# Kernel optimization log

Hardware: AMD Instinct MI355X
Metric: run time of the kernel (lower is better)

The kernel has to match this reference:

```python
import jax, jax.numpy as jnp
import numpy as np

T, N, D, B, L = 4, 1_000_000, 4, 16_384, 50
TOTAL = B * L

def setup_inputs() -> dict:
    key = jax.random.key(0)
    k0, k1, k2, k3, k4 = jax.random.split(key, 5)
    tables = jax.random.normal(k0, (T, N, D), dtype=jnp.float32) * 0.01
    indices = jax.random.randint(k1, (T, TOTAL), 0, N)
    # sorted segment ids encode jagged bag boundaries (variable lengths per sample)
    segment_ids = jnp.sort(jax.random.randint(k2, (T, TOTAL), 0, B), axis=-1)
    W = jax.random.normal(k3, (1, D), dtype=jnp.float32) * (1.0 / np.sqrt(D))
    b = jax.random.normal(k4, (1,), dtype=jnp.float32) * 0.01
    return {"tables": tables, "W": W, "b": b, "indices": indices, "segment_ids": segment_ids}

def reference(tables, W, b, indices, segment_ids):
    # EmbeddingBagCollection: per-table gather + sum pooling over jagged bags
    def pool_one(tbl, idx, seg):
        rows = tbl[idx]                                   # [TOTAL, D] irregular gather
        return jax.ops.segment_sum(rows, seg, num_segments=B)  # [B, D]
    pooled = jax.vmap(pool_one)(tables, indices, segment_ids)  # [T, B, D]
    # to_dict() + per-key append + cat(dim=0)  ==  reshape stacking tables along batch
    sparse_features = pooled.reshape(T * B, D)            # [T*B, D]
    # over_arch Linear(4, 1)
    return sparse_features @ W.T + b                      # [T*B, 1]
```

## Files before the change

### kernel.cpp

```cpp
#include <hip/hip_runtime.h>

constexpr int T     = 4;
constexpr int NROWS = 1000000;
constexpr int B     = 16384;
constexpr int TOTAL = 16384 * 50;

typedef float fv4 __attribute__((ext_vector_type(4)));


__global__ __launch_bounds__(256)
void produce_kernel(const fv4*   __restrict__ tables,
                    const float* __restrict__ Wp,
                    const float* __restrict__ bias,
                    float* __restrict__ p,
                    float* __restrict__ out) {
    const int i = blockIdx.x * 256 + threadIdx.x;
    if (i < T * NROWS) {
        const float wx = Wp[0], wy = Wp[1], wz = Wp[2], ww = Wp[3];
        const fv4 r = tables[i];
        p[i] = r.x * wx + r.y * wy + r.z * wz + r.w * ww;
    }
    if (i < T * B) out[i] = bias[0];
}

__global__ __launch_bounds__(256)
void pool_kernel(const float* __restrict__ p,
                 const int*   __restrict__ indices,
                 const int*   __restrict__ segids,
                 float*       __restrict__ out)
{
    const int xcd    = blockIdx.x & 7;
    const int t      = xcd >> 1;
    const int within = (blockIdx.x >> 3) * 2 + (xcd & 1);
    const int local  = within * 256 + threadIdx.x;
    const int g      = t * TOTAL + local;

    const int lane = threadIdx.x & 63;

    const int seg = __builtin_nontemporal_load(&segids[g]);
    const int idx = __builtin_nontemporal_load(&indices[g]);
    float v = p[t * NROWS + idx];

    #pragma unroll
    for (int d = 1; d < 64; d <<= 1) {
        const float ov = __shfl_up(v, d, 64);
        const int   os = __shfl_up(seg, d, 64);
        if (lane >= d && os == seg) v += ov;
    }

    const int nseg = __shfl_down(seg, 1, 64);
    if (lane == 63 || nseg != seg) {
        atomicAdd(&out[t * B + seg], v);
    }
}

extern "C" void kernel_launch(void* const* d_in, const int* in_sizes, int n_in,
                              void* d_out, int out_size, void* d_ws, size_t ws_size,
                              hipStream_t stream) {
    const fv4*   tables  = (const fv4*)d_in[0];
    const float* W       = (const float*)d_in[1];
    const float* bias    = (const float*)d_in[2];
    const int*   indices = (const int*)d_in[3];
    const int*   segids  = (const int*)d_in[4];
    float*       out     = (float*)d_out;

    float* p = (float*)d_ws;

    {
        int n = T * NROWS;
        produce_kernel<<<(n + 255) / 256, 256, 0, stream>>>(tables, W, bias, p, out);
    }
    {
        pool_kernel<<<12800, 256, 0, stream>>>(p, indices, segids, out);
    }
}
```

Measured before the change: 133.5 us.

## Process four rows per thread in produce and four elements per thread in pool

The produce kernel now has each thread load four table rows with nontemporal 16-byte loads and write four projected values as one vector store. Its blocks use the same XCD-aware mapping from block to table as the pool kernel. The pool kernel reads indices and segment ids as int4 vectors and does a serial segmented prefix over its four elements. It then runs the wave-level shuffle scan on per-thread totals and carries the previous lane's sum into boundary atomics. The goal is fewer threads, wider memory transactions and fewer shuffle rounds per element, at the cost of more intricate carry logic and fewer resident waves to hide gather latency.

```diff
diff --git a/kernel.cpp b/kernel.cpp
--- a/kernel.cpp
+++ b/kernel.cpp
@@ -6,6 +6,7 @@
 constexpr int TOTAL = 16384 * 50;
 
 typedef float fv4 __attribute__((ext_vector_type(4)));
+typedef int   iv4 __attribute__((ext_vector_type(4)));
 
 
 __global__ __launch_bounds__(256)
@@ -14,44 +15,76 @@
                     const float* __restrict__ bias,
                     float* __restrict__ p,
                     float* __restrict__ out) {
-    const int i = blockIdx.x * 256 + threadIdx.x;
-    if (i < T * NROWS) {
+    const int xcd    = blockIdx.x & 7;
+    const int t      = xcd >> 1;
+    const int within = ((blockIdx.x >> 3) << 1) + (xcd & 1);
+    const int r0     = within * 1024 + threadIdx.x * 4;
+
+    if (r0 < NROWS) {
         const float wx = Wp[0], wy = Wp[1], wz = Wp[2], ww = Wp[3];
-        const fv4 r = tables[i];
-        p[i] = r.x * wx + r.y * wy + r.z * wz + r.w * ww;
+        const fv4* src = tables + t * NROWS + r0;
+        const fv4 a = __builtin_nontemporal_load(&src[0]);
+        const fv4 b = __builtin_nontemporal_load(&src[1]);
+        const fv4 c = __builtin_nontemporal_load(&src[2]);
+        const fv4 d = __builtin_nontemporal_load(&src[3]);
+        fv4 res;
+        res.x = a.x * wx + a.y * wy + a.z * wz + a.w * ww;
+        res.y = b.x * wx + b.y * wy + b.z * wz + b.w * ww;
+        res.z = c.x * wx + c.y * wy + c.z * wz + c.w * ww;
+        res.w = d.x * wx + d.y * wy + d.z * wz + d.w * ww;
+        *(fv4*)&p[t * NROWS + r0] = res;
     }
-    if (i < T * B) out[i] = bias[0];
+    const int flat = blockIdx.x * 256 + threadIdx.x;
+    if (flat < T * B) out[flat] = bias[0];
 }
 
 __global__ __launch_bounds__(256)
 void pool_kernel(const float* __restrict__ p,
-                 const int*   __restrict__ indices,
-                 const int*   __restrict__ segids,
+                 const iv4*   __restrict__ indices,
+                 const iv4*   __restrict__ segids,
                  float*       __restrict__ out)
 {
     const int xcd    = blockIdx.x & 7;
     const int t      = xcd >> 1;
-    const int within = (blockIdx.x >> 3) * 2 + (xcd & 1);
-    const int local  = within * 256 + threadIdx.x;
-    const int g      = t * TOTAL + local;
+    const int within = ((blockIdx.x >> 3) << 1) + (xcd & 1);
+    const int q      = within * 256 + threadIdx.x;
+    const int gq     = t * (TOTAL / 4) + q;
+    const int lane   = threadIdx.x & 63;
 
-    const int lane = threadIdx.x & 63;
+    const iv4 s4 = __builtin_nontemporal_load(&segids[gq]);
+    const iv4 i4 = __builtin_nontemporal_load(&indices[gq]);
 
-    const int seg = __builtin_nontemporal_load(&segids[g]);
-    const int idx = __builtin_nontemporal_load(&indices[g]);
-    float v = p[t * NROWS + idx];
+    const float* pt = p + t * NROWS;
+    const float v0 = pt[i4.x];
+    const float v1 = pt[i4.y];
+    const float v2 = pt[i4.z];
+    const float v3 = pt[i4.w];
 
+    const float a0 = v0;
+    const float a1 = v1 + (s4.y == s4.x ? a0 : 0.f);
+    const float a2 = v2 + (s4.z == s4.y ? a1 : 0.f);
+    const float a3 = v3 + (s4.w == s4.z ? a2 : 0.f);
+
+    float x   = a3;
+    int   key = s4.w;
     #pragma unroll
     for (int d = 1; d < 64; d <<= 1) {
-        const float ov = __shfl_up(v, d, 64);
-        const int   os = __shfl_up(seg, d, 64);
-        if (lane >= d && os == seg) v += ov;
+        const float ov = __shfl_up(x, d, 64);
+        const int   ok = __shfl_up(key, d, 64);
+        if (lane >= d && ok == key) x += ov;
     }
 
-    const int nseg = __shfl_down(seg, 1, 64);
-    if (lane == 63 || nseg != seg) {
-        atomicAdd(&out[t * B + seg], v);
-    }
+    const float xprev = __shfl_up(x, 1, 64);
+    const int   kprev = __shfl_up(key, 1, 64);
+    const float carry = (lane > 0 && kprev == s4.x) ? xprev : 0.f;
+
+    float* outt = out + t * B;
+    if (s4.x != s4.y) atomicAdd(&outt[s4.x], a0 + carry);
+    if (s4.y != s4.z) atomicAdd(&outt[s4.y], a1 + (s4.y == s4.x ? carry : 0.f));
+    if (s4.z != s4.w) atomicAdd(&outt[s4.z], a2 + (s4.z == s4.x ? carry : 0.f));
+
+    const int snext = __shfl_down(s4.x, 1, 64);
+    if (lane == 63 || snext != key) atomicAdd(&outt[key], x);
 }
 
 extern "C" void kernel_launch(void* const* d_in, const int* in_sizes, int n_in,
@@ -60,17 +93,12 @@
     const fv4*   tables  = (const fv4*)d_in[0];
     const float* W       = (const float*)d_in[1];
     const float* bias    = (const float*)d_in[2];
-    const int*   indices = (const int*)d_in[3];
-    const int*   segids  = (const int*)d_in[4];
+    const iv4*   indices = (const iv4*)d_in[3];
+    const iv4*   segids  = (const iv4*)d_in[4];
     float*       out     = (float*)d_out;
 
     float* p = (float*)d_ws;
 
-    {
-        int n = T * NROWS;
-        produce_kernel<<<(n + 255) / 256, 256, 0, stream>>>(tables, W, bias, p, out);
-    }
-    {
-        pool_kernel<<<12800, 256, 0, stream>>>(p, indices, segids, out);
-    }
+    produce_kernel<<<3912, 256, 0, stream>>>(tables, W, bias, p, out);
+    pool_kernel<<<3200, 256, 0, stream>>>(p, indices, segids, out);
 }
```

Result: slower. 147.4 us (+10.4%).

## Fuse row projection into gather, dropping full-table precompute pass

Applied to the files above, without the earlier changes.

Removes the pass that projected all 4M table rows onto W into a workspace. The pool kernel now gathers the 16-byte table row directly and computes the dot product per lookup. This avoids streaming 64MB of table data plus writing 16MB of projections. In exchange each random gather fetches 16 bytes instead of 4. Bias initialization moves to a tiny vectorized init kernel.

```diff
diff --git a/kernel.cpp b/kernel.cpp
--- a/kernel.cpp
+++ b/kernel.cpp
@@ -7,31 +7,24 @@
 
 typedef float fv4 __attribute__((ext_vector_type(4)));
 
-
 __global__ __launch_bounds__(256)
-void produce_kernel(const fv4*   __restrict__ tables,
-                    const float* __restrict__ Wp,
-                    const float* __restrict__ bias,
-                    float* __restrict__ p,
-                    float* __restrict__ out) {
+void init_kernel(const float* __restrict__ bias, fv4* __restrict__ out) {
     const int i = blockIdx.x * 256 + threadIdx.x;
-    if (i < T * NROWS) {
-        const float wx = Wp[0], wy = Wp[1], wz = Wp[2], ww = Wp[3];
-        const fv4 r = tables[i];
-        p[i] = r.x * wx + r.y * wy + r.z * wz + r.w * ww;
-    }
-    if (i < T * B) out[i] = bias[0];
+    const float b = bias[0];
+    fv4 v; v.x = b; v.y = b; v.z = b; v.w = b;
+    out[i] = v;
 }
 
 __global__ __launch_bounds__(256)
-void pool_kernel(const float* __restrict__ p,
+void pool_kernel(const fv4*   __restrict__ tables,
+                 const float* __restrict__ Wp,
                  const int*   __restrict__ indices,
                  const int*   __restrict__ segids,
                  float*       __restrict__ out)
 {
     const int xcd    = blockIdx.x & 7;
     const int t      = xcd >> 1;
-    const int within = (blockIdx.x >> 3) * 2 + (xcd & 1);
+    const int within = ((blockIdx.x >> 3) << 1) + (xcd & 1);
     const int local  = within * 256 + threadIdx.x;
     const int g      = t * TOTAL + local;
 
@@ -39,7 +32,10 @@
 
     const int seg = __builtin_nontemporal_load(&segids[g]);
     const int idx = __builtin_nontemporal_load(&indices[g]);
-    float v = p[t * NROWS + idx];
+
+    const fv4 r = tables[t * NROWS + idx];
+    const float wx = Wp[0], wy = Wp[1], wz = Wp[2], ww = Wp[3];
+    float v = r.x * wx + r.y * wy + r.z * wz + r.w * ww;
 
     #pragma unroll
     for (int d = 1; d < 64; d <<= 1) {
@@ -64,13 +60,9 @@
     const int*   segids  = (const int*)d_in[4];
     float*       out     = (float*)d_out;
 
-    float* p = (float*)d_ws;
+    (void)d_ws; (void)ws_size;
 
-    {
-        int n = T * NROWS;
-        produce_kernel<<<(n + 255) / 256, 256, 0, stream>>>(tables, W, bias, p, out);
-    }
-    {
-        pool_kernel<<<12800, 256, 0, stream>>>(p, indices, segids, out);
-    }
+    init_kernel<<<64, 256, 0, stream>>>(bias, (fv4*)out);
+
+    pool_kernel<<<12800, 256, 0, stream>>>(tables, W, indices, segids, out);
 }
```

New measurement: 143.9 us. 7.8% more time.
